# Kernel tuning notes

Hardware: AMD Instinct MI355X
Metric: run time of the kernel (lower is better)

Reference implementation:

```python
import jax, jax.numpy as jnp
import numpy as np

INPUT_DIM, CB_DIM, CB_VOCAB = 512, 16, 8192
N = 16384
EPS = 1e-12  # F.normalize default eps


def setup_inputs() -> dict:
    key = jax.random.key(0)
    kx, kp, kc = jax.random.split(key, 3)
    x = jax.random.normal(kx, (N, INPUT_DIM), dtype=jnp.float32)
    # xavier_uniform_ on P [input_dim, cb_dim]
    bound = float(np.sqrt(6.0 / (INPUT_DIM + CB_DIM)))
    P = jax.random.uniform(kp, (INPUT_DIM, CB_DIM), dtype=jnp.float32,
                           minval=-bound, maxval=bound)
    # CB = F.normalize(randn(cb_vocab, cb_dim)) -> unit rows
    CB = jax.random.normal(kc, (CB_VOCAB, CB_DIM), dtype=jnp.float32)
    CB = CB / jnp.maximum(jnp.linalg.norm(CB, axis=1, keepdims=True), EPS)
    return {"x": x, "P": P, "CB": CB}


def reference(x, P, CB):
    # random projection: [N, input_dim] @ [input_dim, cb_dim] -> [N, cb_dim]
    xp = x @ P
    # L2-normalize projected vectors (rows)
    xp = xp / jnp.maximum(jnp.linalg.norm(xp, axis=1, keepdims=True), EPS)
    # cosine similarity against unit-norm codebook = plain dot product
    sim = xp @ CB.T  # [N, cb_vocab]
    return jnp.argmax(sim, axis=1)  # [N] int codebook indices
```

## Files before the change

### kernel.cpp

```cpp
#include <hip/hip_runtime.h>
#include <stdint.h>

#define N_ROWS   16384
#define IN_DIM   512
#define CB_DIM   16
#define CB_VOCAB 8192

#define PROJ_BLOCKS 1024
#define PREP_BLOCKS 128

#define N_CT   (CB_VOCAB / 16)
#define CODEPARTS 16
#define CT_PER_PART (N_CT / CODEPARTS)
#define N_ROWGRP 64

#define WS_OFF_AFA  0
#define WS_OFF_AFB  (1u << 20)
#define WS_OFF_BHH  (2u << 20)
#define WS_OFF_B31  ((2u << 20) + (512u << 10))
#define WS_OFF_PART (3u << 20)
#define WS_OFF_CNT  ((3u << 20) + (128u << 10))

typedef __attribute__((ext_vector_type(8))) short bf16x8;
typedef __attribute__((ext_vector_type(4))) float f32x4;

__device__ __forceinline__ unsigned fkey(float f) {
    unsigned u = __float_as_uint(f);
    return (u & 0x80000000u) ? ~u : (u | 0x80000000u);
}

__device__ __forceinline__ unsigned short f2bf(float f) {
    unsigned u = __float_as_uint(f);
    return (unsigned short)((u + 0x7FFFu + ((u >> 16) & 1u)) >> 16);
}
__device__ __forceinline__ float bf2f(unsigned short h) {
    return __uint_as_float(((unsigned)h) << 16);
}

__global__ __launch_bounds__(256, 3)
void k_front(const float* __restrict__ x, const float* __restrict__ P,
             const float* __restrict__ CB,
             bf16x8* __restrict__ AfragA, bf16x8* __restrict__ AfragB,
             bf16x8* __restrict__ Bhh, bf16x8* __restrict__ B31,
             unsigned long long* __restrict__ part, unsigned* __restrict__ cnt) {
    __shared__ bf16x8 sPf[3][1024];
    __shared__ __align__(16) float foldb[1024];

    const int tid  = threadIdx.x;
    const int wave = tid >> 6;
    const int lane = tid & 63;

    if (blockIdx.x >= PROJ_BLOCKS) {
        const int pb = blockIdx.x - PROJ_BLOCKS;
        if (tid < 128) part[pb * 128 + tid] = 0ull;
        if (pb == 0 && tid < 64) cnt[tid] = 0u;

        const int ct   = pb * 4 + wave;
        const int n    = lane & 15;
        const int quad = lane >> 4;
        const int kh   = (quad & 1) * 8;
        const int lvl  = quad >> 1;
        const int code = ct * 16 + n;

        const float4* b4 = (const float4*)(CB + (size_t)code * CB_DIM + kh);
        float4 a = b4[0], b = b4[1];
        float v[8] = {a.x, a.y, a.z, a.w, b.x, b.y, b.z, b.w};

        bf16x8 shh, s31;
#pragma unroll
        for (int j = 0; j < 8; ++j) {
            float f = v[j];
            unsigned short b1 = f2bf(f);  float r1 = f - bf2f(b1);
            unsigned short b2 = f2bf(r1); float r2 = r1 - bf2f(b2);
            unsigned short b3 = f2bf(r2);
            shh[j] = (short)(lvl ? b2 : b1);
            s31[j] = (short)(lvl ? b1 : b3);
        }
        Bhh[(size_t)ct * 64 + lane] = shh;
        B31[(size_t)ct * 64 + lane] = s31;
        return;
    }

#pragma unroll
    for (int s4 = 0; s4 < 4; ++s4) {
        const int s  = tid + s4 * 256;
        const int c  = s >> 6;
        const int l  = s & 63;
        const int n  = l & 15;
        const int kq = l >> 4;
        const int k0 = c * 32 + kq * 8;

        bf16x8 p1, p2, p3;
#pragma unroll
        for (int j = 0; j < 8; ++j) {
            float f = P[(size_t)(k0 + j) * CB_DIM + n];
            unsigned short b1 = f2bf(f);  float r1 = f - bf2f(b1);
            unsigned short b2 = f2bf(r1); float r2 = r1 - bf2f(b2);
            unsigned short b3 = f2bf(r2);
            p1[j] = (short)b1; p2[j] = (short)b2; p3[j] = (short)b3;
        }
        sPf[0][s] = p1; sPf[1][s] = p2; sPf[2][s] = p3;
    }
    __syncthreads();

    const int rt = blockIdx.x;
    const int m  = lane & 15;
    const int kq = lane >> 4;
    const float4* xr = (const float4*)(x + (size_t)(rt * 16 + m) * IN_DIM);

    float4 xf[8];
#pragma unroll
    for (int i = 0; i < 4; ++i) {
        xf[2 * i]     = xr[(wave * 4 + i) * 8 + kq * 2];
        xf[2 * i + 1] = xr[(wave * 4 + i) * 8 + kq * 2 + 1];
    }

    f32x4 acc1 = {0.f, 0.f, 0.f, 0.f};
    f32x4 acc2 = {0.f, 0.f, 0.f, 0.f};

#pragma unroll
    for (int i = 0; i < 4; ++i) {
        const int c = wave * 4 + i;
        bf16x8 p1 = sPf[0][c * 64 + lane];
        bf16x8 p2 = sPf[1][c * 64 + lane];
        bf16x8 p3 = sPf[2][c * 64 + lane];

        float4 xa = xf[2 * i], xb = xf[2 * i + 1];
        float xs[8] = {xa.x, xa.y, xa.z, xa.w, xb.x, xb.y, xb.z, xb.w};
        bf16x8 a1, a2, a3;
#pragma unroll
        for (int j = 0; j < 8; ++j) {
            float f = xs[j];
            unsigned short b1 = f2bf(f);  float r1 = f - bf2f(b1);
            unsigned short b2 = f2bf(r1); float r2 = r1 - bf2f(b2);
            unsigned short b3 = f2bf(r2);
            a1[j] = (short)b1; a2[j] = (short)b2; a3[j] = (short)b3;
        }

        acc1 = __builtin_amdgcn_mfma_f32_16x16x32_bf16(a1, p1, acc1, 0, 0, 0);
        acc2 = __builtin_amdgcn_mfma_f32_16x16x32_bf16(a1, p2, acc2, 0, 0, 0);
        acc1 = __builtin_amdgcn_mfma_f32_16x16x32_bf16(a2, p1, acc1, 0, 0, 0);
        acc2 = __builtin_amdgcn_mfma_f32_16x16x32_bf16(a1, p3, acc2, 0, 0, 0);
        acc1 = __builtin_amdgcn_mfma_f32_16x16x32_bf16(a2, p2, acc1, 0, 0, 0);
        acc2 = __builtin_amdgcn_mfma_f32_16x16x32_bf16(a3, p1, acc2, 0, 0, 0);
    }

    *(f32x4*)&foldb[(wave * 64 + lane) * 4] = acc1 + acc2;
    __syncthreads();

    if (wave == 0) {
        f32x4 s0 = *(const f32x4*)&foldb[(0 * 64 + lane) * 4];
        f32x4 s1 = *(const f32x4*)&foldb[(1 * 64 + lane) * 4];
        f32x4 s2 = *(const f32x4*)&foldb[(2 * 64 + lane) * 4];
        f32x4 s3 = *(const f32x4*)&foldb[(3 * 64 + lane) * 4];
        f32x4 sum = ((s0 + s1) + s2) + s3;

        asm volatile("s_waitcnt lgkmcnt(0)" ::: "memory");
        __builtin_amdgcn_sched_barrier(0);

#pragma unroll
        for (int r = 0; r < 4; ++r)
            foldb[(kq * 4 + r) * 20 + m] = sum[r];

        asm volatile("s_waitcnt lgkmcnt(0)" ::: "memory");
        __builtin_amdgcn_sched_barrier(0);

        const int kh  = (kq & 1) * 8;
        const int lvl = kq >> 1;
        bf16x8 sa, sb;
#pragma unroll
        for (int j = 0; j < 8; ++j) {
            float f = foldb[m * 20 + kh + j];
            unsigned short b1 = f2bf(f);  float r1 = f - bf2f(b1);
            unsigned short b2 = f2bf(r1); float r2 = r1 - bf2f(b2);
            unsigned short b3 = f2bf(r2);
            sa[j] = (short)(lvl ? b2 : b1);
            sb[j] = (short)(lvl ? b3 : b1);
        }
        AfragA[(size_t)rt * 64 + lane] = sa;
        AfragB[(size_t)rt * 64 + lane] = sb;
    }
}

__global__ __launch_bounds__(256, 4)
void k_scan(const bf16x8* __restrict__ AfragA, const bf16x8* __restrict__ AfragB,
            const bf16x8* __restrict__ Bhh, const bf16x8* __restrict__ B31,
            unsigned long long* __restrict__ part, unsigned* __restrict__ cnt,
            int* __restrict__ out) {
    __shared__ int s_done;
    const int codepart = blockIdx.x & (CODEPARTS - 1);
    const int rowgrp   = blockIdx.x >> 4;
    const int wave     = threadIdx.x >> 6;
    const int lane     = threadIdx.x & 63;
    const int n        = lane & 15;
    const int quad     = lane >> 4;
    const int rt_base  = rowgrp * 16 + wave * 4;

    bf16x8 Aa[4], Ab[4];
#pragma unroll
    for (int t = 0; t < 4; ++t) {
        Aa[t] = AfragA[(size_t)(rt_base + t) * 64 + lane];
        Ab[t] = AfragB[(size_t)(rt_base + t) * 64 + lane];
    }

    float bestv[4][4];
    int   bestc[4][4];
#pragma unroll
    for (int t = 0; t < 4; ++t)
#pragma unroll
        for (int r = 0; r < 4; ++r) { bestv[t][r] = -INFINITY; bestc[t][r] = 0; }

    const int ct0 = codepart * CT_PER_PART;
    size_t ib = (size_t)ct0 * 64;
    bf16x8 nb1  = Bhh[ib + lane];
    bf16x8 nb1s = Bhh[ib + (lane ^ 32)];
    bf16x8 nb3  = B31[ib + lane];

    for (int c = 0; c < CT_PER_PART; ++c) {
        bf16x8 b1 = nb1, b1s = nb1s, b3 = nb3;
        if (c + 1 < CT_PER_PART) {
            size_t ibn = (size_t)(ct0 + c + 1) * 64;
            nb1  = Bhh[ibn + lane];
            nb1s = Bhh[ibn + (lane ^ 32)];
            nb3  = B31[ibn + lane];
        }
#pragma unroll
        for (int t = 0; t < 4; ++t) {
            f32x4 s = __builtin_amdgcn_mfma_f32_16x16x32_bf16(
                          Aa[t], b1, (f32x4){0.f, 0.f, 0.f, 0.f}, 0, 0, 0);
            s = __builtin_amdgcn_mfma_f32_16x16x32_bf16(Aa[t], b1s, s, 0, 0, 0);
            s = __builtin_amdgcn_mfma_f32_16x16x32_bf16(Ab[t], b3,  s, 0, 0, 0);
#pragma unroll
            for (int r = 0; r < 4; ++r) {
                if (s[r] > bestv[t][r]) { bestv[t][r] = s[r]; bestc[t][r] = c; }
            }
        }
    }

#pragma unroll
    for (int t = 0; t < 4; ++t) {
#pragma unroll
        for (int r = 0; r < 4; ++r) {
            unsigned code = (unsigned)(codepart * 512 + bestc[t][r] * 16 + n);
            unsigned long long packed =
                ((unsigned long long)fkey(bestv[t][r]) << 32) |
                (unsigned long long)(0xFFFFFFFFu - code);
#pragma unroll
            for (int mk = 1; mk <= 8; mk <<= 1) {
                unsigned long long o = __shfl_xor(packed, mk, 64);
                packed = (o > packed) ? o : packed;
            }
            if (n == 0) {
                int row = (rt_base + t) * 16 + quad * 4 + r;
                atomicMax(&part[row], packed);
            }
        }
    }

    __syncthreads();
    if (threadIdx.x == 0)
        s_done = (atomicAdd(&cnt[rowgrp], 1u) == (unsigned)(CODEPARTS - 1));
    __syncthreads();

    if (s_done) {
        int row = rowgrp * 256 + threadIdx.x;
        unsigned long long v = atomicAdd(&part[row], 0ull);
        out[row] = (int)(0xFFFFFFFFu - (unsigned)(v & 0xFFFFFFFFull));
    }
}

extern "C" void kernel_launch(void* const* d_in, const int* in_sizes, int n_in,
                              void* d_out, int out_size, void* d_ws, size_t ws_size,
                              hipStream_t stream) {
    const float* x  = (const float*)d_in[0];
    const float* P  = (const float*)d_in[1];
    const float* CB = (const float*)d_in[2];
    int* out = (int*)d_out;

    char* ws = (char*)d_ws;
    bf16x8* AfragA = (bf16x8*)(ws + WS_OFF_AFA);
    bf16x8* AfragB = (bf16x8*)(ws + WS_OFF_AFB);
    bf16x8* Bhh    = (bf16x8*)(ws + WS_OFF_BHH);
    bf16x8* B31    = (bf16x8*)(ws + WS_OFF_B31);
    unsigned long long* part = (unsigned long long*)(ws + WS_OFF_PART);
    unsigned* cnt  = (unsigned*)(ws + WS_OFF_CNT);

    k_front<<<PROJ_BLOCKS + PREP_BLOCKS, 256, 0, stream>>>(
        x, P, CB, AfragA, AfragB, Bhh, B31, part, cnt);
    k_scan<<<N_ROWGRP * CODEPARTS, 256, 0, stream>>>(
        AfragA, AfragB, Bhh, B31, part, cnt, out);
}
```

Before: 112.6 us.

## Split projection prep into separate kernel and stream P fragments from global

```diff
diff --git a/kernel.cpp b/kernel.cpp
--- a/kernel.cpp
+++ b/kernel.cpp
@@ -6,8 +6,8 @@
 #define CB_DIM   16
 #define CB_VOCAB 8192
 
+#define PREP_BLOCKS 128
 #define PROJ_BLOCKS 1024
-#define PREP_BLOCKS 128
 
 #define N_CT   (CB_VOCAB / 16)
 #define CODEPARTS 16
@@ -20,6 +20,7 @@
 #define WS_OFF_B31  ((2u << 20) + (512u << 10))
 #define WS_OFF_PART (3u << 20)
 #define WS_OFF_CNT  ((3u << 20) + (128u << 10))
+#define WS_OFF_PF   ((3u << 20) + (192u << 10))
 
 typedef __attribute__((ext_vector_type(8))) short bf16x8;
 typedef __attribute__((ext_vector_type(4))) float f32x4;
@@ -37,24 +38,19 @@
     return __uint_as_float(((unsigned)h) << 16);
 }
 
-__global__ __launch_bounds__(256, 3)
-void k_front(const float* __restrict__ x, const float* __restrict__ P,
-             const float* __restrict__ CB,
-             bf16x8* __restrict__ AfragA, bf16x8* __restrict__ AfragB,
-             bf16x8* __restrict__ Bhh, bf16x8* __restrict__ B31,
-             unsigned long long* __restrict__ part, unsigned* __restrict__ cnt) {
-    __shared__ bf16x8 sPf[3][1024];
-    __shared__ __align__(16) float foldb[1024];
-
-    const int tid  = threadIdx.x;
-    const int wave = tid >> 6;
-    const int lane = tid & 63;
-
-    if (blockIdx.x >= PROJ_BLOCKS) {
-        const int pb = blockIdx.x - PROJ_BLOCKS;
-        if (tid < 128) part[pb * 128 + tid] = 0ull;
-        if (pb == 0 && tid < 64) cnt[tid] = 0u;
-
+__global__ __launch_bounds__(256, 2)
+void k_prep(const float* __restrict__ P, const float* __restrict__ CB,
+            bf16x8* __restrict__ Bhh, bf16x8* __restrict__ B31,
+            bf16x8* __restrict__ Pf,
+            unsigned long long* __restrict__ part, unsigned* __restrict__ cnt) {
+    const int pb   = blockIdx.x;
+    const int wave = threadIdx.x >> 6;
+    const int lane = threadIdx.x & 63;
+
+    if (threadIdx.x < 128) part[pb * 128 + threadIdx.x] = 0ull;
+    if (pb == 0 && threadIdx.x < 64) cnt[threadIdx.x] = 0u;
+
+    {
         const int ct   = pb * 4 + wave;
         const int n    = lane & 15;
         const int quad = lane >> 4;
@@ -78,14 +74,12 @@
         }
         Bhh[(size_t)ct * 64 + lane] = shh;
         B31[(size_t)ct * 64 + lane] = s31;
-        return;
-    }
-
-#pragma unroll
-    for (int s4 = 0; s4 < 4; ++s4) {
-        const int s  = tid + s4 * 256;
-        const int c  = s >> 6;
-        const int l  = s & 63;
+    }
+
+    const int gslot = pb * 256 + threadIdx.x;
+    if (gslot < 1024) {
+        const int c  = gslot >> 6;
+        const int l  = gslot & 63;
         const int n  = l & 15;
         const int kq = l >> 4;
         const int k0 = c * 32 + kq * 8;
@@ -99,13 +93,24 @@
             unsigned short b3 = f2bf(r2);
             p1[j] = (short)b1; p2[j] = (short)b2; p3[j] = (short)b3;
         }
-        sPf[0][s] = p1; sPf[1][s] = p2; sPf[2][s] = p3;
-    }
-    __syncthreads();
-
-    const int rt = blockIdx.x;
-    const int m  = lane & 15;
-    const int kq = lane >> 4;
+        Pf[gslot]        = p1;
+        Pf[1024 + gslot] = p2;
+        Pf[2048 + gslot] = p3;
+    }
+}
+
+__global__ __launch_bounds__(256, 4)
+void k_proj(const float* __restrict__ x, const bf16x8* __restrict__ Pf,
+            bf16x8* __restrict__ AfragA, bf16x8* __restrict__ AfragB) {
+    __shared__ __align__(16) float foldb[1024];
+
+    const int tid  = threadIdx.x;
+    const int wave = tid >> 6;
+    const int lane = tid & 63;
+    const int rt   = blockIdx.x;
+    const int m    = lane & 15;
+    const int kq   = lane >> 4;
+
     const float4* xr = (const float4*)(x + (size_t)(rt * 16 + m) * IN_DIM);
 
     float4 xf[8];
@@ -118,12 +123,20 @@
     f32x4 acc1 = {0.f, 0.f, 0.f, 0.f};
     f32x4 acc2 = {0.f, 0.f, 0.f, 0.f};
 
+    const int c0 = wave * 4;
+    bf16x8 p1 = Pf[c0 * 64 + lane];
+    bf16x8 p2 = Pf[1024 + c0 * 64 + lane];
+    bf16x8 p3 = Pf[2048 + c0 * 64 + lane];
+
 #pragma unroll
     for (int i = 0; i < 4; ++i) {
-        const int c = wave * 4 + i;
-        bf16x8 p1 = sPf[0][c * 64 + lane];
-        bf16x8 p2 = sPf[1][c * 64 + lane];
-        bf16x8 p3 = sPf[2][c * 64 + lane];
+        bf16x8 q1, q2, q3;
+        if (i < 3) {
+            const int cn = c0 + i + 1;
+            q1 = Pf[cn * 64 + lane];
+            q2 = Pf[1024 + cn * 64 + lane];
+            q3 = Pf[2048 + cn * 64 + lane];
+        }
 
         float4 xa = xf[2 * i], xb = xf[2 * i + 1];
         float xs[8] = {xa.x, xa.y, xa.z, xa.w, xb.x, xb.y, xb.z, xb.w};
@@ -131,10 +144,15 @@
 #pragma unroll
         for (int j = 0; j < 8; ++j) {
             float f = xs[j];
-            unsigned short b1 = f2bf(f);  float r1 = f - bf2f(b1);
-            unsigned short b2 = f2bf(r1); float r2 = r1 - bf2f(b2);
-            unsigned short b3 = f2bf(r2);
-            a1[j] = (short)b1; a2[j] = (short)b2; a3[j] = (short)b3;
+            unsigned u  = __float_as_uint(f);
+            unsigned h1 = u & 0xFFFF0000u;
+            float r1 = f - __uint_as_float(h1);
+            unsigned u2 = __float_as_uint(r1);
+            unsigned h2 = u2 & 0xFFFF0000u;
+            float r2 = r1 - __uint_as_float(h2);
+            a1[j] = (short)(h1 >> 16);
+            a2[j] = (short)(u2 >> 16);
+            a3[j] = (short)(__float_as_uint(r2) >> 16);
         }
 
         acc1 = __builtin_amdgcn_mfma_f32_16x16x32_bf16(a1, p1, acc1, 0, 0, 0);
@@ -143,6 +161,8 @@
         acc2 = __builtin_amdgcn_mfma_f32_16x16x32_bf16(a1, p3, acc2, 0, 0, 0);
         acc1 = __builtin_amdgcn_mfma_f32_16x16x32_bf16(a2, p2, acc1, 0, 0, 0);
         acc2 = __builtin_amdgcn_mfma_f32_16x16x32_bf16(a3, p1, acc2, 0, 0, 0);
+
+        if (i < 3) { p1 = q1; p2 = q2; p3 = q3; }
     }
 
     *(f32x4*)&foldb[(wave * 64 + lane) * 4] = acc1 + acc2;
@@ -284,9 +304,10 @@
     bf16x8* B31    = (bf16x8*)(ws + WS_OFF_B31);
     unsigned long long* part = (unsigned long long*)(ws + WS_OFF_PART);
     unsigned* cnt  = (unsigned*)(ws + WS_OFF_CNT);
-
-    k_front<<<PROJ_BLOCKS + PREP_BLOCKS, 256, 0, stream>>>(
-        x, P, CB, AfragA, AfragB, Bhh, B31, part, cnt);
+    bf16x8* Pf     = (bf16x8*)(ws + WS_OFF_PF);
+
+    k_prep<<<PREP_BLOCKS, 256, 0, stream>>>(P, CB, Bhh, B31, Pf, part, cnt);
+    k_proj<<<PROJ_BLOCKS, 256, 0, stream>>>(x, Pf, AfragA, AfragB);
     k_scan<<<N_ROWGRP * CODEPARTS, 256, 0, stream>>>(
         AfragA, AfragB, Bhh, B31, part, cnt, out);
 }
```

After: 113.3 us. Within noise of the previous version (+0.6%).
